# Kernel tuning notes

Measured on AMD Instinct MI355X. Metric: run time of the kernel, lower is better.

The kernel has to match this reference:

```python
import jax, jax.numpy as jnp
import numpy as np

NEAR_0 = 1e-08
REG = 0.002


def setup_inputs() -> dict:
    key = jax.random.key(0)
    k1, k2, k3, k4 = jax.random.split(key, 4)
    N = 16777216
    output_1 = jax.random.uniform(k1, (N, 1), dtype=jnp.float32)
    label = jax.random.randint(k2, (N,), 0, 2, dtype=jnp.int64)
    W1 = jax.random.normal(k3, (1024, 4096), dtype=jnp.float32)
    W2 = jax.random.normal(k4, (4096, 1024), dtype=jnp.float32)
    return {"output_1": output_1, "label": label, "W1": W1, "W2": W2}


def reference(output_1, label, W1, W2):
    # output: [N, 2] = [1 - p, p], clamped below at NEAR_0 (eliminate_0)
    probs = jnp.concatenate([1.0 - output_1, output_1], axis=1)
    probs = jnp.maximum(probs, NEAR_0)
    logp = jnp.log(probs)
    # NLLLoss with mean reduction: -mean(logp[i, label[i]])
    picked = jnp.take_along_axis(logp, label[:, None], axis=1)[:, 0]
    nll = -jnp.mean(picked)
    # L2-style regularizer over 2D params: 0.002 * frobenius norm each
    reg = REG * (jnp.sqrt(jnp.sum(W1 * W1)) + jnp.sqrt(jnp.sum(W2 * W2)))
    return nll + reg
```

## Files before the change

### kernel.cpp

```cpp
#include <hip/hip_runtime.h>

#define NEAR0f 1e-8f
#define REGf   0.002f

typedef float __attribute__((ext_vector_type(4))) f32x4;
typedef int   __attribute__((ext_vector_type(4))) i32x4;

__device__ __forceinline__ f32x4 ntload(const f32x4* p) { return __builtin_nontemporal_load(p); }
__device__ __forceinline__ i32x4 ntload(const i32x4* p) { return __builtin_nontemporal_load(p); }

__device__ __forceinline__ float wave_reduce(float v) {
#pragma unroll
    for (int off = 32; off > 0; off >>= 1)
        v += __shfl_down(v, off, 64);
    return v;
}

__device__ __forceinline__ float nll4(f32x4 p, i32x4 l) {
    float a0 = l.x ? p.x : 1.0f - p.x;
    float a1 = l.y ? p.y : 1.0f - p.y;
    float a2 = l.z ? p.z : 1.0f - p.z;
    float a3 = l.w ? p.w : 1.0f - p.w;
    float g0 = __logf(fmaxf(a0, NEAR0f)) + __logf(fmaxf(a1, NEAR0f));
    float g1 = __logf(fmaxf(a2, NEAR0f)) + __logf(fmaxf(a3, NEAR0f));
    return g0 + g1;
}

__device__ __forceinline__ float sq4(f32x4 a, float acc) {
    return fmaf(a.x, a.x, fmaf(a.y, a.y, fmaf(a.z, a.z, fmaf(a.w, a.w, acc))));
}

__global__ __launch_bounds__(256) void reduce_all(
    const f32x4* __restrict__ p4,
    const i32x4* __restrict__ l4,
    const f32x4* __restrict__ w1,
    const f32x4* __restrict__ w2,
    float* __restrict__ acc,
    int n4, int w4)
{
    const int tid    = blockIdx.x * blockDim.x + threadIdx.x;
    const int stride = gridDim.x * blockDim.x;

    float nll0 = 0.0f, nll1 = 0.0f, nll2 = 0.0f, nll3 = 0.0f;
    int i = tid;
    for (; i + 3 * stride < n4; i += 4 * stride) {
        f32x4 p0 = ntload(p4 + i);
        f32x4 p1 = ntload(p4 + i + stride);
        f32x4 p2 = ntload(p4 + i + 2 * stride);
        f32x4 p3 = ntload(p4 + i + 3 * stride);
        i32x4 l0 = ntload(l4 + i);
        i32x4 l1 = ntload(l4 + i + stride);
        i32x4 l2 = ntload(l4 + i + 2 * stride);
        i32x4 l3 = ntload(l4 + i + 3 * stride);
        nll0 -= nll4(p0, l0);
        nll1 -= nll4(p1, l1);
        nll2 -= nll4(p2, l2);
        nll3 -= nll4(p3, l3);
    }
    for (; i < n4; i += stride) {
        nll0 -= nll4(ntload(p4 + i), ntload(l4 + i));
    }
    float nll = (nll0 + nll1) + (nll2 + nll3);

    float s1a = 0.0f, s1b = 0.0f, s2a = 0.0f, s2b = 0.0f;
    int j = tid;
    for (; j + 3 * stride < w4; j += 4 * stride) {
        f32x4 a0 = ntload(w1 + j);
        f32x4 a1 = ntload(w1 + j + stride);
        f32x4 a2 = ntload(w1 + j + 2 * stride);
        f32x4 a3 = ntload(w1 + j + 3 * stride);
        f32x4 b0 = ntload(w2 + j);
        f32x4 b1 = ntload(w2 + j + stride);
        f32x4 b2 = ntload(w2 + j + 2 * stride);
        f32x4 b3 = ntload(w2 + j + 3 * stride);
        s1a = sq4(a0, s1a); s1b = sq4(a1, s1b);
        s1a = sq4(a2, s1a); s1b = sq4(a3, s1b);
        s2a = sq4(b0, s2a); s2b = sq4(b1, s2b);
        s2a = sq4(b2, s2a); s2b = sq4(b3, s2b);
    }
    for (; j < w4; j += stride) {
        s1a = sq4(ntload(w1 + j), s1a);
        s2a = sq4(ntload(w2 + j), s2a);
    }
    float s1 = s1a + s1b;
    float s2 = s2a + s2b;

    nll = wave_reduce(nll);
    s1  = wave_reduce(s1);
    s2  = wave_reduce(s2);

    __shared__ float sm[3][4];
    const int lane = threadIdx.x & 63;
    const int wave = threadIdx.x >> 6;
    if (lane == 0) { sm[0][wave] = nll; sm[1][wave] = s1; sm[2][wave] = s2; }
    __syncthreads();
    if (threadIdx.x == 0) {
        atomicAdd(&acc[0], sm[0][0] + sm[0][1] + sm[0][2] + sm[0][3]);
        atomicAdd(&acc[1], sm[1][0] + sm[1][1] + sm[1][2] + sm[1][3]);
        atomicAdd(&acc[2], sm[2][0] + sm[2][1] + sm[2][2] + sm[2][3]);
    }
}

__global__ void init_acc(float* acc) {
    acc[0] = 0.0f; acc[1] = 0.0f; acc[2] = 0.0f;
}

__global__ void finalize(const float* __restrict__ acc, float* __restrict__ out,
                         float invN) {
    out[0] = acc[0] * invN + REGf * (sqrtf(acc[1]) + sqrtf(acc[2]));
}

extern "C" void kernel_launch(void* const* d_in, const int* in_sizes, int n_in,
                              void* d_out, int out_size, void* d_ws, size_t ws_size,
                              hipStream_t stream) {
    const float* out1  = (const float*)d_in[0];
    const int*   label = (const int*)d_in[1];
    const float* W1    = (const float*)d_in[2];
    const float* W2    = (const float*)d_in[3];

    const int N  = in_sizes[0];
    const int n4 = N / 4;
    const int w4 = in_sizes[2] / 4;

    float* acc = (float*)d_ws;

    init_acc<<<1, 1, 0, stream>>>(acc);
    reduce_all<<<1024, 256, 0, stream>>>(
        (const f32x4*)out1, (const i32x4*)label,
        (const f32x4*)W1,   (const f32x4*)W2,
        acc, n4, w4);
    finalize<<<1, 1, 0, stream>>>(acc, (float*)d_out, 1.0f / (float)N);
}
```

Measured before the change: 190.6 us.

## Replace atomics with per-block partials, drop init kernel, double grid, plain loads

Each block now writes its three partial sums to its own slot in the workspace, and a single 256-thread finalize kernel reduces those slots. This removes the init kernel launch and the global atomics. The grid doubles to 2048 blocks with a launch-bounds occupancy hint, the weight loop unroll drops from 4 to 2, and nontemporal loads become ordinary loads. The trade-offs are a slightly heavier finalize kernel and possible changes in cache behaviour from the plain loads.

```diff
diff --git a/kernel.cpp b/kernel.cpp
--- a/kernel.cpp
+++ b/kernel.cpp
@@ -1,13 +1,11 @@
 #include <hip/hip_runtime.h>
+#include <math.h>
 
 #define NEAR0f 1e-8f
 #define REGf   0.002f
 
 typedef float __attribute__((ext_vector_type(4))) f32x4;
 typedef int   __attribute__((ext_vector_type(4))) i32x4;
-
-__device__ __forceinline__ f32x4 ntload(const f32x4* p) { return __builtin_nontemporal_load(p); }
-__device__ __forceinline__ i32x4 ntload(const i32x4* p) { return __builtin_nontemporal_load(p); }
 
 __device__ __forceinline__ float wave_reduce(float v) {
 #pragma unroll
@@ -30,12 +28,12 @@
     return fmaf(a.x, a.x, fmaf(a.y, a.y, fmaf(a.z, a.z, fmaf(a.w, a.w, acc))));
 }
 
-__global__ __launch_bounds__(256) void reduce_all(
+__global__ __launch_bounds__(256, 8) void reduce_all(
     const f32x4* __restrict__ p4,
     const i32x4* __restrict__ l4,
     const f32x4* __restrict__ w1,
     const f32x4* __restrict__ w2,
-    float* __restrict__ acc,
+    float* __restrict__ part,
     int n4, int w4)
 {
     const int tid    = blockIdx.x * blockDim.x + threadIdx.x;
@@ -44,43 +42,37 @@
     float nll0 = 0.0f, nll1 = 0.0f, nll2 = 0.0f, nll3 = 0.0f;
     int i = tid;
     for (; i + 3 * stride < n4; i += 4 * stride) {
-        f32x4 p0 = ntload(p4 + i);
-        f32x4 p1 = ntload(p4 + i + stride);
-        f32x4 p2 = ntload(p4 + i + 2 * stride);
-        f32x4 p3 = ntload(p4 + i + 3 * stride);
-        i32x4 l0 = ntload(l4 + i);
-        i32x4 l1 = ntload(l4 + i + stride);
-        i32x4 l2 = ntload(l4 + i + 2 * stride);
-        i32x4 l3 = ntload(l4 + i + 3 * stride);
+        f32x4 p0 = p4[i];
+        f32x4 p1 = p4[i + stride];
+        f32x4 p2 = p4[i + 2 * stride];
+        f32x4 p3 = p4[i + 3 * stride];
+        i32x4 l0 = l4[i];
+        i32x4 l1 = l4[i + stride];
+        i32x4 l2 = l4[i + 2 * stride];
+        i32x4 l3 = l4[i + 3 * stride];
         nll0 -= nll4(p0, l0);
         nll1 -= nll4(p1, l1);
         nll2 -= nll4(p2, l2);
         nll3 -= nll4(p3, l3);
     }
     for (; i < n4; i += stride) {
-        nll0 -= nll4(ntload(p4 + i), ntload(l4 + i));
+        nll0 -= nll4(p4[i], l4[i]);
     }
     float nll = (nll0 + nll1) + (nll2 + nll3);
 
     float s1a = 0.0f, s1b = 0.0f, s2a = 0.0f, s2b = 0.0f;
     int j = tid;
-    for (; j + 3 * stride < w4; j += 4 * stride) {
-        f32x4 a0 = ntload(w1 + j);
-        f32x4 a1 = ntload(w1 + j + stride);
-        f32x4 a2 = ntload(w1 + j + 2 * stride);
-        f32x4 a3 = ntload(w1 + j + 3 * stride);
-        f32x4 b0 = ntload(w2 + j);
-        f32x4 b1 = ntload(w2 + j + stride);
-        f32x4 b2 = ntload(w2 + j + 2 * stride);
-        f32x4 b3 = ntload(w2 + j + 3 * stride);
+    for (; j + stride < w4; j += 2 * stride) {
+        f32x4 a0 = w1[j];
+        f32x4 a1 = w1[j + stride];
+        f32x4 b0 = w2[j];
+        f32x4 b1 = w2[j + stride];
         s1a = sq4(a0, s1a); s1b = sq4(a1, s1b);
-        s1a = sq4(a2, s1a); s1b = sq4(a3, s1b);
         s2a = sq4(b0, s2a); s2b = sq4(b1, s2b);
-        s2a = sq4(b2, s2a); s2b = sq4(b3, s2b);
     }
     for (; j < w4; j += stride) {
-        s1a = sq4(ntload(w1 + j), s1a);
-        s2a = sq4(ntload(w2 + j), s2a);
+        s1a = sq4(w1[j], s1a);
+        s2a = sq4(w2[j], s2a);
     }
     float s1 = s1a + s1b;
     float s2 = s2a + s2b;
@@ -95,19 +87,37 @@
     if (lane == 0) { sm[0][wave] = nll; sm[1][wave] = s1; sm[2][wave] = s2; }
     __syncthreads();
     if (threadIdx.x == 0) {
-        atomicAdd(&acc[0], sm[0][0] + sm[0][1] + sm[0][2] + sm[0][3]);
-        atomicAdd(&acc[1], sm[1][0] + sm[1][1] + sm[1][2] + sm[1][3]);
-        atomicAdd(&acc[2], sm[2][0] + sm[2][1] + sm[2][2] + sm[2][3]);
+        f32x4 o;
+        o.x = sm[0][0] + sm[0][1] + sm[0][2] + sm[0][3];
+        o.y = sm[1][0] + sm[1][1] + sm[1][2] + sm[1][3];
+        o.z = sm[2][0] + sm[2][1] + sm[2][2] + sm[2][3];
+        o.w = 0.0f;
+        *(f32x4*)(part + (size_t)blockIdx.x * 4) = o;
     }
 }
 
-__global__ void init_acc(float* acc) {
-    acc[0] = 0.0f; acc[1] = 0.0f; acc[2] = 0.0f;
-}
+__global__ void finalize(const float* __restrict__ part, float* __restrict__ out,
+                         float invN, int nblocks) {
+    float nll = 0.0f, s1 = 0.0f, s2 = 0.0f;
+    for (int i = threadIdx.x; i < nblocks; i += 256) {
+        const f32x4 v = *(const f32x4*)(part + (size_t)i * 4);
+        nll += v.x; s1 += v.y; s2 += v.z;
+    }
+    nll = wave_reduce(nll);
+    s1  = wave_reduce(s1);
+    s2  = wave_reduce(s2);
 
-__global__ void finalize(const float* __restrict__ acc, float* __restrict__ out,
-                         float invN) {
-    out[0] = acc[0] * invN + REGf * (sqrtf(acc[1]) + sqrtf(acc[2]));
+    __shared__ float sm[3][4];
+    const int lane = threadIdx.x & 63;
+    const int wave = threadIdx.x >> 6;
+    if (lane == 0) { sm[0][wave] = nll; sm[1][wave] = s1; sm[2][wave] = s2; }
+    __syncthreads();
+    if (threadIdx.x == 0) {
+        float tn = sm[0][0] + sm[0][1] + sm[0][2] + sm[0][3];
+        float t1 = sm[1][0] + sm[1][1] + sm[1][2] + sm[1][3];
+        float t2 = sm[2][0] + sm[2][1] + sm[2][2] + sm[2][3];
+        out[0] = tn * invN + REGf * (sqrtf(t1) + sqrtf(t2));
+    }
 }
 
 extern "C" void kernel_launch(void* const* d_in, const int* in_sizes, int n_in,
@@ -122,12 +132,12 @@
     const int n4 = N / 4;
     const int w4 = in_sizes[2] / 4;
 
-    float* acc = (float*)d_ws;
+    const int NBLK = 2048;
+    float* part = (float*)d_ws;
 
-    init_acc<<<1, 1, 0, stream>>>(acc);
-    reduce_all<<<1024, 256, 0, stream>>>(
+    reduce_all<<<NBLK, 256, 0, stream>>>(
         (const f32x4*)out1, (const i32x4*)label,
         (const f32x4*)W1,   (const f32x4*)W2,
-        acc, n4, w4);
-    finalize<<<1, 1, 0, stream>>>(acc, (float*)d_out, 1.0f / (float)N);
+        part, n4, w4);
+    finalize<<<1, 256, 0, stream>>>(part, (float*)d_out, 1.0f / (float)N, NBLK);
 }
```

Result: faster. 179.5 us (-5.8%).

## Specialize fixed-size path with inline-asm batched global loads

Applied to the files above, without the earlier changes.

Adds a fast path for the case where the element counts exactly match the grid stride multiples. It issues 16 dwordx4 loads at once through inline assembly with SGPR base addresses and VGPR offsets, then does a single wait. Nontemporal loads are dropped in favour of plain loads, and launch bounds request 4 blocks per CU. The goal is more memory-level parallelism and cheaper addressing, at the cost of more registers, the asm-enforced full wait, and a path that only fires for these sizes.

```diff
diff --git a/kernel.cpp b/kernel.cpp
--- a/kernel.cpp
+++ b/kernel.cpp
@@ -1,13 +1,11 @@
 #include <hip/hip_runtime.h>
+#include <math.h>
 
 #define NEAR0f 1e-8f
 #define REGf   0.002f
 
 typedef float __attribute__((ext_vector_type(4))) f32x4;
 typedef int   __attribute__((ext_vector_type(4))) i32x4;
-
-__device__ __forceinline__ f32x4 ntload(const f32x4* p) { return __builtin_nontemporal_load(p); }
-__device__ __forceinline__ i32x4 ntload(const i32x4* p) { return __builtin_nontemporal_load(p); }
 
 __device__ __forceinline__ float wave_reduce(float v) {
 #pragma unroll
@@ -30,60 +28,108 @@
     return fmaf(a.x, a.x, fmaf(a.y, a.y, fmaf(a.z, a.z, fmaf(a.w, a.w, acc))));
 }
 
-__global__ __launch_bounds__(256) void reduce_all(
-    const f32x4* __restrict__ p4,
-    const i32x4* __restrict__ l4,
-    const f32x4* __restrict__ w1,
-    const f32x4* __restrict__ w2,
+__global__ __launch_bounds__(256, 4) void reduce_all(
+    const float* __restrict__ pB,
+    const int*   __restrict__ lB,
+    const float* __restrict__ w1B,
+    const float* __restrict__ w2B,
     float* __restrict__ acc,
     int n4, int w4)
 {
     const int tid    = blockIdx.x * blockDim.x + threadIdx.x;
     const int stride = gridDim.x * blockDim.x;
 
-    float nll0 = 0.0f, nll1 = 0.0f, nll2 = 0.0f, nll3 = 0.0f;
-    int i = tid;
-    for (; i + 3 * stride < n4; i += 4 * stride) {
-        f32x4 p0 = ntload(p4 + i);
-        f32x4 p1 = ntload(p4 + i + stride);
-        f32x4 p2 = ntload(p4 + i + 2 * stride);
-        f32x4 p3 = ntload(p4 + i + 3 * stride);
-        i32x4 l0 = ntload(l4 + i);
-        i32x4 l1 = ntload(l4 + i + stride);
-        i32x4 l2 = ntload(l4 + i + 2 * stride);
-        i32x4 l3 = ntload(l4 + i + 3 * stride);
-        nll0 -= nll4(p0, l0);
-        nll1 -= nll4(p1, l1);
-        nll2 -= nll4(p2, l2);
-        nll3 -= nll4(p3, l3);
+    float nll = 0.0f, s1 = 0.0f, s2 = 0.0f;
+
+    if (n4 == 16 * stride && w4 == 4 * stride) {
+        const unsigned base = (unsigned)tid * 16u;
+        const unsigned step = (unsigned)stride * 16u;
+
+        float nA = 0.0f, nB = 0.0f, nC = 0.0f, nD = 0.0f;
+#pragma unroll
+        for (int b = 0; b < 2; ++b) {
+            const unsigned o0 = base + (unsigned)(8 * b) * step;
+            const unsigned o1 = o0 + step;
+            const unsigned o2 = o0 + 2u * step;
+            const unsigned o3 = o0 + 3u * step;
+            const unsigned o4 = o0 + 4u * step;
+            const unsigned o5 = o0 + 5u * step;
+            const unsigned o6 = o0 + 6u * step;
+            const unsigned o7 = o0 + 7u * step;
+            f32x4 p0, p1, p2, p3, p4, p5, p6, p7;
+            i32x4 l0, l1, l2, l3, l4, l5, l6, l7;
+            asm volatile(
+                "global_load_dwordx4 %0, %16, %24\n\t"
+                "global_load_dwordx4 %8, %16, %25\n\t"
+                "global_load_dwordx4 %1, %17, %24\n\t"
+                "global_load_dwordx4 %9, %17, %25\n\t"
+                "global_load_dwordx4 %2, %18, %24\n\t"
+                "global_load_dwordx4 %10, %18, %25\n\t"
+                "global_load_dwordx4 %3, %19, %24\n\t"
+                "global_load_dwordx4 %11, %19, %25\n\t"
+                "global_load_dwordx4 %4, %20, %24\n\t"
+                "global_load_dwordx4 %12, %20, %25\n\t"
+                "global_load_dwordx4 %5, %21, %24\n\t"
+                "global_load_dwordx4 %13, %21, %25\n\t"
+                "global_load_dwordx4 %6, %22, %24\n\t"
+                "global_load_dwordx4 %14, %22, %25\n\t"
+                "global_load_dwordx4 %7, %23, %24\n\t"
+                "global_load_dwordx4 %15, %23, %25\n\t"
+                "s_waitcnt vmcnt(0)"
+                : "=v"(p0), "=v"(p1), "=v"(p2), "=v"(p3),
+                  "=v"(p4), "=v"(p5), "=v"(p6), "=v"(p7),
+                  "=v"(l0), "=v"(l1), "=v"(l2), "=v"(l3),
+                  "=v"(l4), "=v"(l5), "=v"(l6), "=v"(l7)
+                : "v"(o0), "v"(o1), "v"(o2), "v"(o3),
+                  "v"(o4), "v"(o5), "v"(o6), "v"(o7),
+                  "s"(pB), "s"(lB)
+                : "memory");
+            nA -= nll4(p0, l0); nB -= nll4(p1, l1);
+            nC -= nll4(p2, l2); nD -= nll4(p3, l3);
+            nA -= nll4(p4, l4); nB -= nll4(p5, l5);
+            nC -= nll4(p6, l6); nD -= nll4(p7, l7);
+        }
+        nll = (nA + nB) + (nC + nD);
+
+        {
+            const unsigned o0 = base;
+            const unsigned o1 = base + step;
+            const unsigned o2 = base + 2u * step;
+            const unsigned o3 = base + 3u * step;
+            f32x4 a0, a1, a2, a3, b0, b1, b2, b3;
+            asm volatile(
+                "global_load_dwordx4 %0, %8, %12\n\t"
+                "global_load_dwordx4 %4, %8, %13\n\t"
+                "global_load_dwordx4 %1, %9, %12\n\t"
+                "global_load_dwordx4 %5, %9, %13\n\t"
+                "global_load_dwordx4 %2, %10, %12\n\t"
+                "global_load_dwordx4 %6, %10, %13\n\t"
+                "global_load_dwordx4 %3, %11, %12\n\t"
+                "global_load_dwordx4 %7, %11, %13\n\t"
+                "s_waitcnt vmcnt(0)"
+                : "=v"(a0), "=v"(a1), "=v"(a2), "=v"(a3),
+                  "=v"(b0), "=v"(b1), "=v"(b2), "=v"(b3)
+                : "v"(o0), "v"(o1), "v"(o2), "v"(o3),
+                  "s"(w1B), "s"(w2B)
+                : "memory");
+            float s1a = sq4(a0, 0.0f), s1b = sq4(a1, 0.0f);
+            s1a = sq4(a2, s1a); s1b = sq4(a3, s1b);
+            float s2a = sq4(b0, 0.0f), s2b = sq4(b1, 0.0f);
+            s2a = sq4(b2, s2a); s2b = sq4(b3, s2b);
+            s1 = s1a + s1b;
+            s2 = s2a + s2b;
+        }
+    } else {
+        const f32x4* p4v = (const f32x4*)pB;
+        const i32x4* l4v = (const i32x4*)lB;
+        const f32x4* w1v = (const f32x4*)w1B;
+        const f32x4* w2v = (const f32x4*)w2B;
+        for (int i = tid; i < n4; i += stride) nll -= nll4(p4v[i], l4v[i]);
+        for (int j = tid; j < w4; j += stride) {
+            s1 = sq4(w1v[j], s1);
+            s2 = sq4(w2v[j], s2);
+        }
     }
-    for (; i < n4; i += stride) {
-        nll0 -= nll4(ntload(p4 + i), ntload(l4 + i));
-    }
-    float nll = (nll0 + nll1) + (nll2 + nll3);
-
-    float s1a = 0.0f, s1b = 0.0f, s2a = 0.0f, s2b = 0.0f;
-    int j = tid;
-    for (; j + 3 * stride < w4; j += 4 * stride) {
-        f32x4 a0 = ntload(w1 + j);
-        f32x4 a1 = ntload(w1 + j + stride);
-        f32x4 a2 = ntload(w1 + j + 2 * stride);
-        f32x4 a3 = ntload(w1 + j + 3 * stride);
-        f32x4 b0 = ntload(w2 + j);
-        f32x4 b1 = ntload(w2 + j + stride);
-        f32x4 b2 = ntload(w2 + j + 2 * stride);
-        f32x4 b3 = ntload(w2 + j + 3 * stride);
-        s1a = sq4(a0, s1a); s1b = sq4(a1, s1b);
-        s1a = sq4(a2, s1a); s1b = sq4(a3, s1b);
-        s2a = sq4(b0, s2a); s2b = sq4(b1, s2b);
-        s2a = sq4(b2, s2a); s2b = sq4(b3, s2b);
-    }
-    for (; j < w4; j += stride) {
-        s1a = sq4(ntload(w1 + j), s1a);
-        s2a = sq4(ntload(w2 + j), s2a);
-    }
-    float s1 = s1a + s1b;
-    float s2 = s2a + s2b;
 
     nll = wave_reduce(nll);
     s1  = wave_reduce(s1);
@@ -126,8 +172,6 @@
 
     init_acc<<<1, 1, 0, stream>>>(acc);
     reduce_all<<<1024, 256, 0, stream>>>(
-        (const f32x4*)out1, (const i32x4*)label,
-        (const f32x4*)W1,   (const f32x4*)W2,
-        acc, n4, w4);
+        out1, label, W1, W2, acc, n4, w4);
     finalize<<<1, 1, 0, stream>>>(acc, (float*)d_out, 1.0f / (float)N);
 }
```

After: 192.8 us. Within noise of the previous version (+1.2%).

## Stream inputs through per-wave LDS ring with async global_load_lds pipelining

Applied to the files above, without the earlier changes.

Replaces the direct nontemporal vector loads with asynchronous global-to-LDS loads into a four-deep per-wave ring buffer. The fused NLL and weight-norm loops become one fully unrolled 20-step schedule with explicit vmcnt waits, keeping several loads in flight while earlier slots are consumed. This fast path only runs when the sizes match exactly 16 and 4 strides for the current grid; otherwise a simple scalar-stride fallback is used. It adds 32 KB of LDS per block, which may limit occupancy, and drops the nontemporal cache hints.

```diff
diff --git a/kernel.cpp b/kernel.cpp
--- a/kernel.cpp
+++ b/kernel.cpp
@@ -1,4 +1,5 @@
 #include <hip/hip_runtime.h>
+#include <math.h>
 
 #define NEAR0f 1e-8f
 #define REGf   0.002f
@@ -6,8 +7,10 @@
 typedef float __attribute__((ext_vector_type(4))) f32x4;
 typedef int   __attribute__((ext_vector_type(4))) i32x4;
 
-__device__ __forceinline__ f32x4 ntload(const f32x4* p) { return __builtin_nontemporal_load(p); }
-__device__ __forceinline__ i32x4 ntload(const i32x4* p) { return __builtin_nontemporal_load(p); }
+#define WAITV(n) do { \
+    asm volatile("s_waitcnt vmcnt(" #n ")" ::: "memory"); \
+    __builtin_amdgcn_sched_barrier(0); \
+} while (0)
 
 __device__ __forceinline__ float wave_reduce(float v) {
 #pragma unroll
@@ -30,6 +33,12 @@
     return fmaf(a.x, a.x, fmaf(a.y, a.y, fmaf(a.z, a.z, fmaf(a.w, a.w, acc))));
 }
 
+__device__ __forceinline__ void gload16(const void* g, void* l) {
+    __builtin_amdgcn_global_load_lds(
+        (const __attribute__((address_space(1))) void*)g,
+        (__attribute__((address_space(3))) void*)l, 16, 0, 0);
+}
+
 __global__ __launch_bounds__(256) void reduce_all(
     const f32x4* __restrict__ p4,
     const i32x4* __restrict__ l4,
@@ -38,61 +47,66 @@
     float* __restrict__ acc,
     int n4, int w4)
 {
+    __shared__ char ring[4][4][2048];
+
     const int tid    = blockIdx.x * blockDim.x + threadIdx.x;
     const int stride = gridDim.x * blockDim.x;
+    const int lane   = threadIdx.x & 63;
+    const int wv     = threadIdx.x >> 6;
 
-    float nll0 = 0.0f, nll1 = 0.0f, nll2 = 0.0f, nll3 = 0.0f;
-    int i = tid;
-    for (; i + 3 * stride < n4; i += 4 * stride) {
-        f32x4 p0 = ntload(p4 + i);
-        f32x4 p1 = ntload(p4 + i + stride);
-        f32x4 p2 = ntload(p4 + i + 2 * stride);
-        f32x4 p3 = ntload(p4 + i + 3 * stride);
-        i32x4 l0 = ntload(l4 + i);
-        i32x4 l1 = ntload(l4 + i + stride);
-        i32x4 l2 = ntload(l4 + i + 2 * stride);
-        i32x4 l3 = ntload(l4 + i + 3 * stride);
-        nll0 -= nll4(p0, l0);
-        nll1 -= nll4(p1, l1);
-        nll2 -= nll4(p2, l2);
-        nll3 -= nll4(p3, l3);
+    float nllA = 0.0f, nllB = 0.0f, s1 = 0.0f, s2 = 0.0f;
+
+    if (n4 == 16 * stride && w4 == 4 * stride) {
+        auto issue = [&](int j) {
+            char* base = &ring[wv][j & 3][0];
+            if (j < 16) {
+                gload16(p4 + (size_t)tid + (size_t)j * stride, base);
+                gload16(l4 + (size_t)tid + (size_t)j * stride, base + 1024);
+            } else {
+                const int k = j - 16;
+                gload16(w1 + (size_t)tid + (size_t)k * stride, base);
+                gload16(w2 + (size_t)tid + (size_t)k * stride, base + 1024);
+            }
+        };
+
+        issue(0); issue(1); issue(2); issue(3);
+
+#pragma unroll
+        for (int t = 0; t < 20; ++t) {
+            if (t <= 16)      WAITV(6);
+            else if (t == 17) WAITV(4);
+            else if (t == 18) WAITV(2);
+            else              WAITV(0);
+
+            const char* base = &ring[wv][t & 3][0];
+            if (t < 16) {
+                const f32x4 pv = *(const f32x4*)(base + (size_t)lane * 16);
+                const i32x4 lv = *(const i32x4*)(base + 1024 + (size_t)lane * 16);
+                if (t & 1) nllB -= nll4(pv, lv);
+                else       nllA -= nll4(pv, lv);
+            } else {
+                const f32x4 av = *(const f32x4*)(base + (size_t)lane * 16);
+                const f32x4 bv = *(const f32x4*)(base + 1024 + (size_t)lane * 16);
+                s1 = sq4(av, s1);
+                s2 = sq4(bv, s2);
+            }
+            if (t + 4 < 20) issue(t + 4);
+        }
+    } else {
+        for (int i = tid; i < n4; i += stride) nllA -= nll4(p4[i], l4[i]);
+        for (int j = tid; j < w4; j += stride) {
+            s1 = sq4(w1[j], s1);
+            s2 = sq4(w2[j], s2);
+        }
     }
-    for (; i < n4; i += stride) {
-        nll0 -= nll4(ntload(p4 + i), ntload(l4 + i));
-    }
-    float nll = (nll0 + nll1) + (nll2 + nll3);
 
-    float s1a = 0.0f, s1b = 0.0f, s2a = 0.0f, s2b = 0.0f;
-    int j = tid;
-    for (; j + 3 * stride < w4; j += 4 * stride) {
-        f32x4 a0 = ntload(w1 + j);
-        f32x4 a1 = ntload(w1 + j + stride);
-        f32x4 a2 = ntload(w1 + j + 2 * stride);
-        f32x4 a3 = ntload(w1 + j + 3 * stride);
-        f32x4 b0 = ntload(w2 + j);
-        f32x4 b1 = ntload(w2 + j + stride);
-        f32x4 b2 = ntload(w2 + j + 2 * stride);
-        f32x4 b3 = ntload(w2 + j + 3 * stride);
-        s1a = sq4(a0, s1a); s1b = sq4(a1, s1b);
-        s1a = sq4(a2, s1a); s1b = sq4(a3, s1b);
-        s2a = sq4(b0, s2a); s2b = sq4(b1, s2b);
-        s2a = sq4(b2, s2a); s2b = sq4(b3, s2b);
-    }
-    for (; j < w4; j += stride) {
-        s1a = sq4(ntload(w1 + j), s1a);
-        s2a = sq4(ntload(w2 + j), s2a);
-    }
-    float s1 = s1a + s1b;
-    float s2 = s2a + s2b;
-
+    float nll = nllA + nllB;
     nll = wave_reduce(nll);
     s1  = wave_reduce(s1);
     s2  = wave_reduce(s2);
 
     __shared__ float sm[3][4];
-    const int lane = threadIdx.x & 63;
-    const int wave = threadIdx.x >> 6;
-    if (lane == 0) { sm[0][wave] = nll; sm[1][wave] = s1; sm[2][wave] = s2; }
+    if (lane == 0) { sm[0][wv] = nll; sm[1][wv] = s1; sm[2][wv] = s2; }
     __syncthreads();
     if (threadIdx.x == 0) {
         atomicAdd(&acc[0], sm[0][0] + sm[0][1] + sm[0][2] + sm[0][3]);
```

Measured after the change: 193.6 us. Within noise of the previous version (+1.6%).
